# Optimization experiments

Measured on AMD Instinct MI355X. Metric: run time of the kernel, lower is better.

The kernel has to match this reference:

```python
import jax, jax.numpy as jnp
import numpy as np

B, S, E, H = 4, 1024, 1024, 16
D = E // H          # head_dim = 64
ROT = 32            # rotary dims (first ROT channels of each head)


def _rope(x, freqs):
    # x: [B, H, S, D]; freqs: [1, 1, S, ROT]
    r = freqs.shape[-1]
    xl, xr = x[..., :r], x[..., r:]
    half = r // 2
    rot = jnp.concatenate([-xl[..., half:], xl[..., :half]], axis=-1)  # rotate_half
    xl = xl * jnp.cos(freqs) + rot * jnp.sin(freqs)
    return jnp.concatenate([xl, xr], axis=-1)


def setup_inputs() -> dict:
    key = jax.random.key(0)
    ks = jax.random.split(key, 7)
    std = 0.02
    return {
        "hidden_states": jax.random.normal(ks[0], (B, S, E), jnp.float32),
        "rotary_pos_emb": jax.random.normal(ks[1], (1, S, ROT), jnp.float32),
        "q_w": jax.random.normal(ks[2], (E, E), jnp.float32) * std,
        "k_w": jax.random.normal(ks[3], (E, E), jnp.float32) * std,
        "v_w": jax.random.normal(ks[4], (E, E), jnp.float32) * std,
        "o_w": jax.random.normal(ks[5], (E, E), jnp.float32) * std,
        "o_b": jnp.zeros((E,), jnp.float32),
    }


def reference(hidden_states, rotary_pos_emb, q_w, k_w, v_w, o_w, o_b):
    bsz, tgt_len, embed_dim = hidden_states.shape
    scale = D ** -0.5

    def shape(t):  # [B, S, E] -> [B, H, S, D]
        return t.reshape(bsz, tgt_len, H, D).transpose(0, 2, 1, 3)

    q = shape(hidden_states @ q_w.T * scale)
    k = shape(hidden_states @ k_w.T)
    v = shape(hidden_states @ v_w.T)

    freqs = rotary_pos_emb[:, None, :, :]  # [1, 1, S, ROT]
    q = _rope(q, freqs)
    k = _rope(k, freqs)
    v = _rope(v, freqs)

    attn = jnp.einsum("bhqd,bhkd->bhqk", q, k)
    causal = jnp.tril(jnp.ones((tgt_len, tgt_len), bool))
    attn = jnp.where(causal, attn, jnp.finfo(attn.dtype).min)
    attn = jax.nn.softmax(attn, axis=-1)

    out = jnp.einsum("bhqk,bhkd->bhqd", attn, v)
    out = out.transpose(0, 2, 1, 3).reshape(bsz, tgt_len, embed_dim)
    return out @ o_w.T + o_b
```

## Files before the change

kernel.cpp:

```cpp
#include <hip/hip_runtime.h>
#include <hip/hip_bf16.h>

typedef __bf16 bf16;
typedef __attribute__((ext_vector_type(2))) __bf16 bf16x2;
typedef __attribute__((ext_vector_type(4))) __bf16 bf16x4;
typedef __attribute__((ext_vector_type(8))) __bf16 bf16x8;
typedef __attribute__((ext_vector_type(4))) float f32x4;

#define NB 4
#define NS 1024
#define NE 1024
#define NH 16
#define ND 64
#define NROT 32
#define NM (NB*NS)

__device__ __forceinline__ void gload_lds16(const bf16* g, void* l) {
  __builtin_amdgcn_global_load_lds(
      (const __attribute__((address_space(1))) unsigned int*)g,
      (__attribute__((address_space(3))) unsigned int*)l,
      16, 0, 0);
}

__global__ void k_cvt(const float* __restrict__ src, bf16* __restrict__ dst, int n4) {
  int i = blockIdx.x * 256 + threadIdx.x;
  if (i >= n4) return;
  float4 v = reinterpret_cast<const float4*>(src)[i];
  bf16x4 o = { (bf16)v.x, (bf16)v.y, (bf16)v.z, (bf16)v.w };
  *reinterpret_cast<bf16x4*>(dst + (size_t)i * 4) = o;
}

struct Cvt4Args {
  const float* s0; const float* s1; const float* s2; const float* s3;
  bf16* d0; bf16* d1; bf16* d2; bf16* d3;
};
__global__ void k_cvt4(Cvt4Args a, int n4) {
  const float* s; bf16* d;
  switch (blockIdx.y) {
    case 0:  s = a.s0; d = a.d0; break;
    case 1:  s = a.s1; d = a.d1; break;
    case 2:  s = a.s2; d = a.d2; break;
    default: s = a.s3; d = a.d3; break;
  }
  int i = blockIdx.x * 256 + threadIdx.x;
  if (i >= n4) return;
  float4 v = reinterpret_cast<const float4*>(s)[i];
  bf16x4 o = { (bf16)v.x, (bf16)v.y, (bf16)v.z, (bf16)v.w };
  *reinterpret_cast<bf16x4*>(d + (size_t)i * 4) = o;
}

__global__ void k_tab(const float* __restrict__ rot, float* __restrict__ ct,
                      float* __restrict__ st, int n) {
  int i = blockIdx.x * 256 + threadIdx.x;
  if (i >= n) return;
  float v = rot[i];
  ct[i] = cosf(v);
  st[i] = sinf(v);
}

template<int BM, int BN, bool SWAP>
__device__ __forceinline__ void gemm_core(
    const bf16* __restrict__ A, const bf16* __restrict__ W,
    bf16* lA, bf16* lB, int m0, int n0, f32x4 (&acc)[BM/32][BN/32])
{
  const int tid = threadIdx.x;
  const int wave = tid >> 6, lane = tid & 63;
  const int wm = wave >> 1, wn = wave & 1;
  const int fr = lane & 15, kg = lane >> 4;
  const int lrow8 = lane >> 3, lslot = lane & 7;

  for (int kt = 0; kt < NE; kt += 64) {
#pragma unroll
    for (int i = 0; i < BM / 32; ++i) {
      int chunk = i * 4 + wave;
      int row = (chunk << 3) + lrow8;
      int slot = lslot ^ (row & 7);
      gload_lds16(A + (size_t)(m0 + row) * NE + kt + slot * 8, (char*)lA + chunk * 1024);
    }
#pragma unroll
    for (int i = 0; i < BN / 32; ++i) {
      int chunk = i * 4 + wave;
      int row = (chunk << 3) + lrow8;
      int slot = lslot ^ (row & 7);
      gload_lds16(W + (size_t)(n0 + row) * NE + kt + slot * 8, (char*)lB + chunk * 1024);
    }
    __syncthreads();
#pragma unroll
    for (int kk = 0; kk < 2; ++kk) {
      bf16x8 af[BM / 32], bfr[BN / 32];
#pragma unroll
      for (int i = 0; i < BM / 32; ++i) {
        int ra = wm * (BM / 2) + i * 16 + fr;
        af[i] = *reinterpret_cast<const bf16x8*>(lA + ra * 64 + (((kg + 4 * kk) ^ (ra & 7)) << 3));
      }
#pragma unroll
      for (int j = 0; j < BN / 32; ++j) {
        int rb = wn * (BN / 2) + j * 16 + fr;
        bfr[j] = *reinterpret_cast<const bf16x8*>(lB + rb * 64 + (((kg + 4 * kk) ^ (rb & 7)) << 3));
      }
#pragma unroll
      for (int i = 0; i < BM / 32; ++i)
#pragma unroll
        for (int j = 0; j < BN / 32; ++j) {
          if constexpr (SWAP)
            acc[j][i] = __builtin_amdgcn_mfma_f32_16x16x32_bf16(bfr[j], af[i], acc[j][i], 0, 0, 0);
          else
            acc[i][j] = __builtin_amdgcn_mfma_f32_16x16x32_bf16(af[i], bfr[j], acc[i][j], 0, 0, 0);
        }
    }
    __syncthreads();
  }
}

__global__ __launch_bounds__(256) void k_gemm_qk(
    const bf16* __restrict__ A, const bf16* __restrict__ Wq, const bf16* __restrict__ Wk,
    bf16* __restrict__ Oq, bf16* __restrict__ Ok,
    const float* __restrict__ ct, const float* __restrict__ st)
{
  __shared__ bf16 lA[128 * 64];
  __shared__ bf16 lB[128 * 64];
  const int z = blockIdx.z;
  const bf16* W = (z == 0) ? Wq : Wk;
  bf16* Og = (z == 0) ? Oq : Ok;
  const float scale = (z == 0) ? 0.125f * 1.44269504f : 1.0f;
  const int m0 = blockIdx.x * 128, n0 = blockIdx.y * 128;

  f32x4 acc[4][4] = {};
  gemm_core<128, 128, false>(A, W, lA, lB, m0, n0, acc);

  const int tid = threadIdx.x;
  const int wave = tid >> 6, lane = tid & 63;
  const int wm = wave >> 1, wn = wave & 1;
  const int fr = lane & 15, kg = lane >> 4;

#pragma unroll
  for (int i = 0; i < 4; ++i) {
    int rowbase = m0 + wm * 64 + i * 16 + kg * 4;
#pragma unroll
    for (int r = 0; r < 4; ++r) {
      int gm = rowbase + r;
      int s = gm & (NS - 1);
      float x0 = acc[i][0][r] * scale;
      float x1 = acc[i][1][r] * scale;
      float c0 = ct[s * NROT + fr],      sn0 = st[s * NROT + fr];
      float c1 = ct[s * NROT + 16 + fr], sn1 = st[s * NROT + 16 + fr];
      float y0 = x0 * c0 - x1 * sn0;
      float y1 = x1 * c1 + x0 * sn1;
      size_t rb = (size_t)gm * NE + n0 + wn * 64;
      Og[rb + 0 * 16 + fr] = (bf16)y0;
      Og[rb + 1 * 16 + fr] = (bf16)y1;
      Og[rb + 2 * 16 + fr] = (bf16)(acc[i][2][r] * scale);
      Og[rb + 3 * 16 + fr] = (bf16)(acc[i][3][r] * scale);
    }
  }
}

__global__ __launch_bounds__(256) void k_gemm_vt(
    const bf16* __restrict__ A, const bf16* __restrict__ W, bf16* __restrict__ vt,
    const float* __restrict__ ct, const float* __restrict__ st)
{
  __shared__ bf16 lA[128 * 64];
  __shared__ bf16 lB[128 * 64];
  const int m0 = blockIdx.x * 128, n0 = blockIdx.y * 128;
  f32x4 acc[4][4] = {};
  gemm_core<128, 128, true>(A, W, lA, lB, m0, n0, acc);

  const int tid = threadIdx.x;
  const int wave = tid >> 6, lane = tid & 63;
  const int wm = wave >> 1, wn = wave & 1;
  const int fr = lane & 15, kg = lane >> 4;
  const int b = m0 >> 10;
  const int h = (n0 + wn * 64) >> 6;
  bf16* vtb = vt + ((size_t)(b * 16 + h)) * ND * NS;

#pragma unroll
  for (int i = 0; i < 4; ++i) {
    int sl = (m0 & (NS - 1)) + wm * 64 + i * 16 + fr;
#pragma unroll
    for (int r = 0; r < 4; ++r) {
      int dbase = kg * 4 + r;
      float x0 = acc[0][i][r];
      float x1 = acc[1][i][r];
      float c0 = ct[sl * NROT + dbase],      sn0 = st[sl * NROT + dbase];
      float c1 = ct[sl * NROT + 16 + dbase], sn1 = st[sl * NROT + 16 + dbase];
      float y0 = x0 * c0 - x1 * sn0;
      float y1 = x1 * c1 + x0 * sn1;
      vtb[(size_t)(dbase)      * NS + sl] = (bf16)y0;
      vtb[(size_t)(16 + dbase) * NS + sl] = (bf16)y1;
      vtb[(size_t)(32 + dbase) * NS + sl] = (bf16)acc[2][i][r];
      vtb[(size_t)(48 + dbase) * NS + sl] = (bf16)acc[3][i][r];
    }
  }
}

__global__ __launch_bounds__(256) void k_gemm_o(
    const bf16* __restrict__ A, const bf16* __restrict__ W, float* __restrict__ Og,
    const float* __restrict__ bias)
{
  __shared__ bf16 lA[64 * 64];
  __shared__ bf16 lB[128 * 64];
  const int m0 = blockIdx.x * 64, n0 = blockIdx.y * 128;
  f32x4 acc[2][4] = {};
  gemm_core<64, 128, false>(A, W, lA, lB, m0, n0, acc);

  const int tid = threadIdx.x;
  const int wave = tid >> 6, lane = tid & 63;
  const int wm = wave >> 1, wn = wave & 1;
  const int fr = lane & 15, kg = lane >> 4;
#pragma unroll
  for (int i = 0; i < 2; ++i)
#pragma unroll
    for (int j = 0; j < 4; ++j) {
      int gc = n0 + wn * 64 + j * 16 + fr;
      float bv = bias[gc];
#pragma unroll
      for (int r = 0; r < 4; ++r) {
        int gm = m0 + wm * 32 + i * 16 + kg * 4 + r;
        Og[(size_t)gm * NE + gc] = acc[i][j][r] + bv;
      }
    }
}

__global__ __launch_bounds__(256) void k_attn(
    const bf16* __restrict__ Q, const bf16* __restrict__ K,
    const bf16* __restrict__ VT, bf16* __restrict__ O)
{
  __shared__ bf16 lK[2][64 * 64];
  __shared__ bf16 lVT[64 * 64];
  __shared__ bf16 lP[4][16 * 68];
  const int tid = threadIdx.x;
  const int wave = tid >> 6, lane = tid & 63;
  const int fr = lane & 15, kg = lane >> 4;

  const int qt = 15 - (blockIdx.y >> 3);
  const int bh = blockIdx.x | ((blockIdx.y & 7) << 3);
  const int b = bh >> 4, h = bh & 15;
  const int nt = qt + 1;
  const bf16* Qb  = Q + (size_t)b * NS * NE + h * 64;
  const bf16* Kb  = K + (size_t)b * NS * NE + h * 64;
  const bf16* VTb = VT + (size_t)bh * ND * NS;
  bf16* Ob = O + (size_t)b * NS * NE + h * 64;

  const int qrow0 = qt * 64 + wave * 16;

  bf16x8 qf[2];
#pragma unroll
  for (int kk = 0; kk < 2; ++kk)
    qf[kk] = *reinterpret_cast<const bf16x8*>(
        Qb + (size_t)(qrow0 + fr) * NE + kk * 32 + kg * 8);

  const int srow = lane >> 3;
  const int sslot = (lane & 7) ^ srow;
  const int r0 = wave * 8 + srow;
  const int r1 = (wave + 4) * 8 + srow;
  const bf16* kA0 = Kb + (size_t)r0 * NE + sslot * 8;
  const bf16* kA1 = Kb + (size_t)r1 * NE + sslot * 8;
  const bf16* vA0 = VTb + (size_t)r0 * NS + sslot * 8;
  const bf16* vA1 = VTb + (size_t)r1 * NS + sslot * 8;
  char* ldsK0a = (char*)lK[0] + wave * 1024;
  char* ldsK0b = (char*)lK[0] + (wave + 4) * 1024;
  char* ldsK1a = (char*)lK[1] + wave * 1024;
  char* ldsK1b = (char*)lK[1] + (wave + 4) * 1024;
  char* ldsVa  = (char*)lVT + wave * 1024;
  char* ldsVb  = (char*)lVT + (wave + 4) * 1024;

  float m_ = -3.0e38f, l_ = 0.f;
  f32x4 oacc[4] = {};

  gload_lds16(kA0, ldsK0a);
  gload_lds16(kA1, ldsK0b);
  __syncthreads();

  for (int t = 0; t < nt; ++t) {
    const int c = t & 1;
    gload_lds16(vA0 + t * 64, ldsVa);
    gload_lds16(vA1 + t * 64, ldsVb);

    const bf16* lKc = lK[c];
    f32x4 sacc[4] = {};
    __builtin_amdgcn_s_setprio(1);
#pragma unroll
    for (int kk = 0; kk < 2; ++kk)
#pragma unroll
      for (int j = 0; j < 4; ++j) {
        int rc = j * 16 + fr;
        bf16x8 kf = *reinterpret_cast<const bf16x8*>(
            lKc + rc * 64 + (((kg + 4 * kk) ^ (rc & 7)) << 3));
        sacc[j] = __builtin_amdgcn_mfma_f32_16x16x32_bf16(kf, qf[kk], sacc[j], 0, 0, 0);
      }
    __builtin_amdgcn_s_setprio(0);

    if (t == qt) {
      const int ql = wave * 16 + fr;
#pragma unroll
      for (int j = 0; j < 4; ++j)
#pragma unroll
        for (int r = 0; r < 4; ++r)
          if (16 * j + 4 * kg + r > ql) sacc[j][r] = -3.0e38f;
    }

    float m4 = fmaxf(fmaxf(fmaxf(sacc[0][0], sacc[0][1]), fmaxf(sacc[0][2], sacc[0][3])),
                     fmaxf(fmaxf(sacc[1][0], sacc[1][1]), fmaxf(sacc[1][2], sacc[1][3])));
    m4 = fmaxf(m4, fmaxf(fmaxf(fmaxf(sacc[2][0], sacc[2][1]), fmaxf(sacc[2][2], sacc[2][3])),
                         fmaxf(fmaxf(sacc[3][0], sacc[3][1]), fmaxf(sacc[3][2], sacc[3][3]))));
    m4 = fmaxf(m4, __shfl_xor(m4, 16));
    m4 = fmaxf(m4, __shfl_xor(m4, 32));

    if (!__all(m4 - m_ <= 8.0f)) {
      float nm = fmaxf(m_, m4);
      float corr = exp2f(m_ - nm);
      m_ = nm;
      l_ *= corr;
#pragma unroll
      for (int r = 0; r < 4; ++r) {
        float cr = __shfl(corr, kg * 4 + r);
#pragma unroll
        for (int df = 0; df < 4; ++df) oacc[df][r] *= cr;
      }
    }

    float ps = 0.f;
#pragma unroll
    for (int j = 0; j < 4; ++j) {
      float p0 = exp2f(sacc[j][0] - m_);
      float p1 = exp2f(sacc[j][1] - m_);
      float p2 = exp2f(sacc[j][2] - m_);
      float p3 = exp2f(sacc[j][3] - m_);
      ps += (p0 + p1) + (p2 + p3);
      bf16x4 pp = { (bf16)p0, (bf16)p1, (bf16)p2, (bf16)p3 };
      *reinterpret_cast<bf16x4*>(&lP[wave][fr * 68 + j * 16 + kg * 4]) = pp;
    }
    ps += __shfl_xor(ps, 16);
    ps += __shfl_xor(ps, 32);
    l_ += ps;

    __syncthreads();

    if (t + 1 < nt) {
      const bf16* ka = kA0 + (size_t)(t + 1) * 64 * NE;
      const bf16* kb2 = kA1 + (size_t)(t + 1) * 64 * NE;
      if (c) { gload_lds16(ka, ldsK0a); gload_lds16(kb2, ldsK0b); }
      else   { gload_lds16(ka, ldsK1a); gload_lds16(kb2, ldsK1b); }
    }

    __builtin_amdgcn_s_setprio(1);
#pragma unroll
    for (int ks = 0; ks < 2; ++ks) {
      bf16x8 pf = *reinterpret_cast<const bf16x8*>(&lP[wave][fr * 68 + ks * 32 + kg * 8]);
#pragma unroll
      for (int df = 0; df < 4; ++df) {
        int d = df * 16 + fr;
        bf16x8 vf = *reinterpret_cast<const bf16x8*>(
            (const bf16*)lVT + d * 64 + (((kg + 4 * ks) ^ (d & 7)) << 3));
        oacc[df] = __builtin_amdgcn_mfma_f32_16x16x32_bf16(pf, vf, oacc[df], 0, 0, 0);
      }
    }
    __builtin_amdgcn_s_setprio(0);

    __syncthreads();
  }

  float linv[4];
#pragma unroll
  for (int r = 0; r < 4; ++r) linv[r] = 1.0f / __shfl(l_, kg * 4 + r);
#pragma unroll
  for (int df = 0; df < 4; ++df)
#pragma unroll
    for (int r = 0; r < 4; ++r)
      Ob[(size_t)(qrow0 + kg * 4 + r) * NE + df * 16 + fr] = (bf16)(oacc[df][r] * linv[r]);
}

extern "C" void kernel_launch(void* const* d_in, const int* in_sizes, int n_in,
                              void* d_out, int out_size, void* d_ws, size_t ws_size,
                              hipStream_t stream) {
  const float* hs  = (const float*)d_in[0];
  const float* rot = (const float*)d_in[1];
  const float* qw  = (const float*)d_in[2];
  const float* kw  = (const float*)d_in[3];
  const float* vw  = (const float*)d_in[4];
  const float* ow  = (const float*)d_in[5];
  const float* obb = (const float*)d_in[6];
  float* out = (float*)d_out;

  char* ws = (char*)d_ws;
  size_t off = 0;
  bf16* hb  = (bf16*)(ws + off); off += (size_t)NM * NE * 2;
  bf16* wqb = (bf16*)(ws + off); off += (size_t)NE * NE * 2;
  bf16* wkb = (bf16*)(ws + off); off += (size_t)NE * NE * 2;
  bf16* wvb = (bf16*)(ws + off); off += (size_t)NE * NE * 2;
  bf16* wob = (bf16*)(ws + off); off += (size_t)NE * NE * 2;
  bf16* qb  = (bf16*)(ws + off); off += (size_t)NM * NE * 2;
  bf16* kb  = (bf16*)(ws + off); off += (size_t)NM * NE * 2;
  bf16* vt  = (bf16*)(ws + off); off += (size_t)NM * NE * 2;
  float* ct = (float*)(ws + off); off += (size_t)NS * NROT * 4;
  float* st = (float*)(ws + off); off += (size_t)NS * NROT * 4;
  bf16* aob = hb;

  k_cvt<<<dim3((NM * NE / 4 + 255) / 256), dim3(256), 0, stream>>>(hs, hb, NM * NE / 4);
  Cvt4Args ca = { qw, kw, vw, ow, wqb, wkb, wvb, wob };
  k_cvt4<<<dim3(NE * NE / 4 / 256, 4), dim3(256), 0, stream>>>(ca, NE * NE / 4);
  k_tab<<<dim3((NS * NROT + 255) / 256), dim3(256), 0, stream>>>(rot, ct, st, NS * NROT);

  k_gemm_qk<<<dim3(NM / 128, NE / 128, 2), dim3(256), 0, stream>>>(
      hb, wqb, wkb, qb, kb, ct, st);
  k_gemm_vt<<<dim3(NM / 128, NE / 128), dim3(256), 0, stream>>>(hb, wvb, vt, ct, st);

  k_attn<<<dim3(8, 128), dim3(256), 0, stream>>>(qb, kb, vt, aob);

  k_gemm_o<<<dim3(NM / 64, NE / 128), dim3(256), 0, stream>>>(aob, wob, out, obb);

  (void)in_sizes; (void)n_in; (void)out_size; (void)ws_size;
}
```

Baseline: 104.4 us.

## Merge prep and projection launches; issue next K tile prefetch earlier in attention

The three conversion and rotary-table kernels become one grid-partitioned prep kernel. The Q/K and V projection GEMMs become a single launch indexed by blockIdx.z, which cuts launch gaps and gives the GPU one larger grid with less tail imbalance. In the attention loop, the next K tile is now prefetched at the start of each iteration, alongside the V load, instead of after the softmax barrier. This overlaps the K load with the QK MFMAs and softmax, at the cost of more loads in flight together with the V tile.

```diff
diff --git a/kernel.cpp b/kernel.cpp
--- a/kernel.cpp
+++ b/kernel.cpp
@@ -22,40 +22,33 @@
       16, 0, 0);
 }
 
-__global__ void k_cvt(const float* __restrict__ src, bf16* __restrict__ dst, int n4) {
-  int i = blockIdx.x * 256 + threadIdx.x;
-  if (i >= n4) return;
-  float4 v = reinterpret_cast<const float4*>(src)[i];
-  bf16x4 o = { (bf16)v.x, (bf16)v.y, (bf16)v.z, (bf16)v.w };
-  *reinterpret_cast<bf16x4*>(dst + (size_t)i * 4) = o;
-}
-
-struct Cvt4Args {
-  const float* s0; const float* s1; const float* s2; const float* s3;
-  bf16* d0; bf16* d1; bf16* d2; bf16* d3;
+struct PrepArgs {
+  const float* w0; const float* w1; const float* w2; const float* w3;
+  bf16* b0; bf16* b1; bf16* b2; bf16* b3;
+  const float* hs; bf16* hb;
+  const float* rot; float* ct; float* st;
 };
-__global__ void k_cvt4(Cvt4Args a, int n4) {
-  const float* s; bf16* d;
-  switch (blockIdx.y) {
-    case 0:  s = a.s0; d = a.d0; break;
-    case 1:  s = a.s1; d = a.d1; break;
-    case 2:  s = a.s2; d = a.d2; break;
-    default: s = a.s3; d = a.d3; break;
+__global__ void k_prep(PrepArgs a) {
+  const int y = blockIdx.y;
+  const int i = blockIdx.x * 256 + threadIdx.x;
+  if (y < 4) {
+    const float* s = (y == 0) ? a.w0 : (y == 1) ? a.w1 : (y == 2) ? a.w2 : a.w3;
+    bf16* d = (y == 0) ? a.b0 : (y == 1) ? a.b1 : (y == 2) ? a.b2 : a.b3;
+    float4 v = reinterpret_cast<const float4*>(s)[i];
+    bf16x4 o = { (bf16)v.x, (bf16)v.y, (bf16)v.z, (bf16)v.w };
+    *reinterpret_cast<bf16x4*>(d + (size_t)i * 4) = o;
+  } else if (y < 8) {
+    size_t off = (size_t)(y - 4) * (NM * NE / 16);
+    float4 v = reinterpret_cast<const float4*>(a.hs)[off + i];
+    bf16x4 o = { (bf16)v.x, (bf16)v.y, (bf16)v.z, (bf16)v.w };
+    *reinterpret_cast<bf16x4*>(a.hb + (off + i) * 4) = o;
+  } else {
+    if (i < NS * NROT) {
+      float v = a.rot[i];
+      a.ct[i] = cosf(v);
+      a.st[i] = sinf(v);
+    }
   }
-  int i = blockIdx.x * 256 + threadIdx.x;
-  if (i >= n4) return;
-  float4 v = reinterpret_cast<const float4*>(s)[i];
-  bf16x4 o = { (bf16)v.x, (bf16)v.y, (bf16)v.z, (bf16)v.w };
-  *reinterpret_cast<bf16x4*>(d + (size_t)i * 4) = o;
-}
-
-__global__ void k_tab(const float* __restrict__ rot, float* __restrict__ ct,
-                      float* __restrict__ st, int n) {
-  int i = blockIdx.x * 256 + threadIdx.x;
-  if (i >= n) return;
-  float v = rot[i];
-  ct[i] = cosf(v);
-  st[i] = sinf(v);
 }
 
 template<int BM, int BN, bool SWAP>
@@ -112,83 +105,72 @@
   }
 }
 
-__global__ __launch_bounds__(256) void k_gemm_qk(
+__global__ __launch_bounds__(256) void k_proj(
     const bf16* __restrict__ A, const bf16* __restrict__ Wq, const bf16* __restrict__ Wk,
-    bf16* __restrict__ Oq, bf16* __restrict__ Ok,
-    const float* __restrict__ ct, const float* __restrict__ st)
+    const bf16* __restrict__ Wv, bf16* __restrict__ Oq, bf16* __restrict__ Ok,
+    bf16* __restrict__ vt, const float* __restrict__ ct, const float* __restrict__ st)
 {
   __shared__ bf16 lA[128 * 64];
   __shared__ bf16 lB[128 * 64];
   const int z = blockIdx.z;
-  const bf16* W = (z == 0) ? Wq : Wk;
-  bf16* Og = (z == 0) ? Oq : Ok;
-  const float scale = (z == 0) ? 0.125f * 1.44269504f : 1.0f;
   const int m0 = blockIdx.x * 128, n0 = blockIdx.y * 128;
-
-  f32x4 acc[4][4] = {};
-  gemm_core<128, 128, false>(A, W, lA, lB, m0, n0, acc);
-
   const int tid = threadIdx.x;
   const int wave = tid >> 6, lane = tid & 63;
   const int wm = wave >> 1, wn = wave & 1;
   const int fr = lane & 15, kg = lane >> 4;
 
-#pragma unroll
-  for (int i = 0; i < 4; ++i) {
-    int rowbase = m0 + wm * 64 + i * 16 + kg * 4;
-#pragma unroll
-    for (int r = 0; r < 4; ++r) {
-      int gm = rowbase + r;
-      int s = gm & (NS - 1);
-      float x0 = acc[i][0][r] * scale;
-      float x1 = acc[i][1][r] * scale;
-      float c0 = ct[s * NROT + fr],      sn0 = st[s * NROT + fr];
-      float c1 = ct[s * NROT + 16 + fr], sn1 = st[s * NROT + 16 + fr];
-      float y0 = x0 * c0 - x1 * sn0;
-      float y1 = x1 * c1 + x0 * sn1;
-      size_t rb = (size_t)gm * NE + n0 + wn * 64;
-      Og[rb + 0 * 16 + fr] = (bf16)y0;
-      Og[rb + 1 * 16 + fr] = (bf16)y1;
-      Og[rb + 2 * 16 + fr] = (bf16)(acc[i][2][r] * scale);
-      Og[rb + 3 * 16 + fr] = (bf16)(acc[i][3][r] * scale);
-    }
-  }
-}
-
-__global__ __launch_bounds__(256) void k_gemm_vt(
-    const bf16* __restrict__ A, const bf16* __restrict__ W, bf16* __restrict__ vt,
-    const float* __restrict__ ct, const float* __restrict__ st)
-{
-  __shared__ bf16 lA[128 * 64];
-  __shared__ bf16 lB[128 * 64];
-  const int m0 = blockIdx.x * 128, n0 = blockIdx.y * 128;
-  f32x4 acc[4][4] = {};
-  gemm_core<128, 128, true>(A, W, lA, lB, m0, n0, acc);
-
-  const int tid = threadIdx.x;
-  const int wave = tid >> 6, lane = tid & 63;
-  const int wm = wave >> 1, wn = wave & 1;
-  const int fr = lane & 15, kg = lane >> 4;
-  const int b = m0 >> 10;
-  const int h = (n0 + wn * 64) >> 6;
-  bf16* vtb = vt + ((size_t)(b * 16 + h)) * ND * NS;
-
-#pragma unroll
-  for (int i = 0; i < 4; ++i) {
-    int sl = (m0 & (NS - 1)) + wm * 64 + i * 16 + fr;
-#pragma unroll
-    for (int r = 0; r < 4; ++r) {
-      int dbase = kg * 4 + r;
-      float x0 = acc[0][i][r];
-      float x1 = acc[1][i][r];
-      float c0 = ct[sl * NROT + dbase],      sn0 = st[sl * NROT + dbase];
-      float c1 = ct[sl * NROT + 16 + dbase], sn1 = st[sl * NROT + 16 + dbase];
-      float y0 = x0 * c0 - x1 * sn0;
-      float y1 = x1 * c1 + x0 * sn1;
-      vtb[(size_t)(dbase)      * NS + sl] = (bf16)y0;
-      vtb[(size_t)(16 + dbase) * NS + sl] = (bf16)y1;
-      vtb[(size_t)(32 + dbase) * NS + sl] = (bf16)acc[2][i][r];
-      vtb[(size_t)(48 + dbase) * NS + sl] = (bf16)acc[3][i][r];
+  if (z == 2) {
+    f32x4 acc[4][4] = {};
+    gemm_core<128, 128, true>(A, Wv, lA, lB, m0, n0, acc);
+
+    const int b = m0 >> 10;
+    const int h = (n0 + wn * 64) >> 6;
+    bf16* vtb = vt + ((size_t)(b * 16 + h)) * ND * NS;
+#pragma unroll
+    for (int i = 0; i < 4; ++i) {
+      int sl = (m0 & (NS - 1)) + wm * 64 + i * 16 + fr;
+#pragma unroll
+      for (int r = 0; r < 4; ++r) {
+        int dbase = kg * 4 + r;
+        float x0 = acc[0][i][r];
+        float x1 = acc[1][i][r];
+        float c0 = ct[sl * NROT + dbase],      sn0 = st[sl * NROT + dbase];
+        float c1 = ct[sl * NROT + 16 + dbase], sn1 = st[sl * NROT + 16 + dbase];
+        float y0 = x0 * c0 - x1 * sn0;
+        float y1 = x1 * c1 + x0 * sn1;
+        vtb[(size_t)(dbase)      * NS + sl] = (bf16)y0;
+        vtb[(size_t)(16 + dbase) * NS + sl] = (bf16)y1;
+        vtb[(size_t)(32 + dbase) * NS + sl] = (bf16)acc[2][i][r];
+        vtb[(size_t)(48 + dbase) * NS + sl] = (bf16)acc[3][i][r];
+      }
+    }
+  } else {
+    const bf16* W = (z == 0) ? Wq : Wk;
+    bf16* Og = (z == 0) ? Oq : Ok;
+    const float scale = (z == 0) ? 0.125f * 1.44269504f : 1.0f;
+
+    f32x4 acc[4][4] = {};
+    gemm_core<128, 128, false>(A, W, lA, lB, m0, n0, acc);
+
+#pragma unroll
+    for (int i = 0; i < 4; ++i) {
+      int rowbase = m0 + wm * 64 + i * 16 + kg * 4;
+#pragma unroll
+      for (int r = 0; r < 4; ++r) {
+        int gm = rowbase + r;
+        int s = gm & (NS - 1);
+        float x0 = acc[i][0][r] * scale;
+        float x1 = acc[i][1][r] * scale;
+        float c0 = ct[s * NROT + fr],      sn0 = st[s * NROT + fr];
+        float c1 = ct[s * NROT + 16 + fr], sn1 = st[s * NROT + 16 + fr];
+        float y0 = x0 * c0 - x1 * sn0;
+        float y1 = x1 * c1 + x0 * sn1;
+        size_t rb = (size_t)gm * NE + n0 + wn * 64;
+        Og[rb + 0 * 16 + fr] = (bf16)y0;
+        Og[rb + 1 * 16 + fr] = (bf16)y1;
+        Og[rb + 2 * 16 + fr] = (bf16)(acc[i][2][r] * scale);
+        Og[rb + 3 * 16 + fr] = (bf16)(acc[i][3][r] * scale);
+      }
     }
   }
 }
@@ -257,24 +239,26 @@
   const bf16* kA1 = Kb + (size_t)r1 * NE + sslot * 8;
   const bf16* vA0 = VTb + (size_t)r0 * NS + sslot * 8;
   const bf16* vA1 = VTb + (size_t)r1 * NS + sslot * 8;
-  char* ldsK0a = (char*)lK[0] + wave * 1024;
-  char* ldsK0b = (char*)lK[0] + (wave + 4) * 1024;
-  char* ldsK1a = (char*)lK[1] + wave * 1024;
-  char* ldsK1b = (char*)lK[1] + (wave + 4) * 1024;
+  char* ldsKa[2] = { (char*)lK[0] + wave * 1024, (char*)lK[1] + wave * 1024 };
+  char* ldsKb[2] = { (char*)lK[0] + (wave + 4) * 1024, (char*)lK[1] + (wave + 4) * 1024 };
   char* ldsVa  = (char*)lVT + wave * 1024;
   char* ldsVb  = (char*)lVT + (wave + 4) * 1024;
 
   float m_ = -3.0e38f, l_ = 0.f;
   f32x4 oacc[4] = {};
 
-  gload_lds16(kA0, ldsK0a);
-  gload_lds16(kA1, ldsK0b);
+  gload_lds16(kA0, ldsKa[0]);
+  gload_lds16(kA1, ldsKb[0]);
   __syncthreads();
 
   for (int t = 0; t < nt; ++t) {
     const int c = t & 1;
     gload_lds16(vA0 + t * 64, ldsVa);
     gload_lds16(vA1 + t * 64, ldsVb);
+    if (t + 1 < nt) {
+      gload_lds16(kA0 + (size_t)(t + 1) * 64 * NE, ldsKa[c ^ 1]);
+      gload_lds16(kA1 + (size_t)(t + 1) * 64 * NE, ldsKb[c ^ 1]);
+    }
 
     const bf16* lKc = lK[c];
     f32x4 sacc[4] = {};
@@ -335,13 +319,6 @@
     l_ += ps;
 
     __syncthreads();
-
-    if (t + 1 < nt) {
-      const bf16* ka = kA0 + (size_t)(t + 1) * 64 * NE;
-      const bf16* kb2 = kA1 + (size_t)(t + 1) * 64 * NE;
-      if (c) { gload_lds16(ka, ldsK0a); gload_lds16(kb2, ldsK0b); }
-      else   { gload_lds16(ka, ldsK1a); gload_lds16(kb2, ldsK1b); }
-    }
 
     __builtin_amdgcn_s_setprio(1);
 #pragma unroll
@@ -396,14 +373,11 @@
   float* st = (float*)(ws + off); off += (size_t)NS * NROT * 4;
   bf16* aob = hb;
 
-  k_cvt<<<dim3((NM * NE / 4 + 255) / 256), dim3(256), 0, stream>>>(hs, hb, NM * NE / 4);
-  Cvt4Args ca = { qw, kw, vw, ow, wqb, wkb, wvb, wob };
-  k_cvt4<<<dim3(NE * NE / 4 / 256, 4), dim3(256), 0, stream>>>(ca, NE * NE / 4);
-  k_tab<<<dim3((NS * NROT + 255) / 256), dim3(256), 0, stream>>>(rot, ct, st, NS * NROT);
-
-  k_gemm_qk<<<dim3(NM / 128, NE / 128, 2), dim3(256), 0, stream>>>(
-      hb, wqb, wkb, qb, kb, ct, st);
-  k_gemm_vt<<<dim3(NM / 128, NE / 128), dim3(256), 0, stream>>>(hb, wvb, vt, ct, st);
+  PrepArgs pa = { qw, kw, vw, ow, wqb, wkb, wvb, wob, hs, hb, rot, ct, st };
+  k_prep<<<dim3(NE * NE / 4 / 256, 9), dim3(256), 0, stream>>>(pa);
+
+  k_proj<<<dim3(NM / 128, NE / 128, 3), dim3(256), 0, stream>>>(
+      hb, wqb, wkb, wvb, qb, kb, vt, ct, st);
 
   k_attn<<<dim3(8, 128), dim3(256), 0, stream>>>(qb, kb, vt, aob);
 
```

Result: faster. 98.12 us (-6.0%).
